# Optimization experiments

Measured on AMD Instinct MI355X. Metric: run time of the kernel, lower is better.

The kernel has to match this reference:

```python
import jax, jax.numpy as jnp
import numpy as np


def _orthogonalize(Wfree):
    # Wfree: (S, C, C) free parameters -> batched QR with sign correction
    Q, R = jnp.linalg.qr(Wfree)
    s = jnp.sign(jnp.diagonal(R, axis1=-2, axis2=-1))  # (S, C)
    s = jnp.where(s == 0, jnp.ones_like(s), s)
    return Q * s[:, None, :]  # column-wise sign fix


def _channel_mix(x, Wfree):
    # x: (B, C, H, W); Wfree: (H*W, C, C)
    B, C, H, Wd = x.shape
    S = H * Wd
    Q = _orthogonalize(Wfree)                      # (S, C, C)
    xr = x.reshape(B, C, S).transpose(0, 2, 1)     # (B, S, C)
    # y[b,s,:] = x[b,s,:] @ Q[s].T  (matches torch matmul(x, Q.T))
    y = jnp.einsum('bsk,sck->bsc', xr, Q)
    return y.transpose(0, 2, 1).reshape(B, C, H, Wd)


def setup_inputs() -> dict:
    key = jax.random.key(0)
    k0, k1, k2, k3 = jax.random.split(key, 4)
    init_scale = 0.001
    x0 = jax.random.normal(k0, (32, 64, 28, 28), dtype=jnp.float32)
    x1 = jax.random.normal(k1, (32, 256, 14, 14), dtype=jnp.float32)
    W0 = jax.random.normal(k2, (28 * 28, 64, 64), dtype=jnp.float32) * init_scale
    W1 = jax.random.normal(k3, (14 * 14, 256, 256), dtype=jnp.float32) * init_scale
    return {"x0": x0, "x1": x1, "W0": W0, "W1": W1}


def reference(x0, x1, W0, W1):
    # C=64 and C=256 are perfect squares, so channel padding is a no-op.
    y0 = _channel_mix(x0, W0)
    y1 = _channel_mix(x1, W1)
    return (y0, y1)
```

## Files before the change

kernel.cpp:

```cpp
#include <hip/hip_runtime.h>


static constexpr int BB = 32;

#define SCHED_FENCE() __builtin_amdgcn_sched_barrier(0)

template<int CTRL>
__device__ __forceinline__ float dpp_add(float x) {
    int y = __builtin_amdgcn_update_dpp(0, __float_as_int(x), CTRL, 0xF, 0xF, false);
    return x + __int_as_float(y);
}
__device__ __forceinline__ float rowred16(float p) {
    p = dpp_add<0x128>(p);
    p = dpp_add<0x124>(p);
    p = dpp_add<0x122>(p);
    p = dpp_add<0x121>(p);
    return p;
}

__device__ __forceinline__ int qoff(int j, int g, int r16) {
    return j * 256 + g * 64 + ((r16 ^ (2 * g)) << 2);
}

__global__ __launch_bounds__(256) void tkern(const float* __restrict__ in,
                                             float* __restrict__ out,
                                             int R, int S) {
    __shared__ float tile[32][33];
    const int tx = threadIdx.x, ty = threadIdx.y;
    const int s0 = blockIdx.x * 32, r0 = blockIdx.y * 32;
    #pragma unroll
    for (int i = ty; i < 32; i += 8) {
        int r = r0 + i, s = s0 + tx;
        tile[i][tx] = (r < R && s < S) ? in[(size_t)r * S + s] : 0.f;
    }
    __syncthreads();
    #pragma unroll
    for (int i = ty; i < 32; i += 8) {
        int s = s0 + i, r = r0 + tx;
        if (s < S && r < R) out[(size_t)s * R + r] = tile[tx][i];
    }
}

template<int C, int CT, int KC>
__device__ __forceinline__ void qr_body(const float* __restrict__ W,
                                        float* __restrict__ XY) {
    constexpr int RT = 16;
    constexpr int TR = C / RT;
    constexpr int THREADS = RT * CT;
    constexpr int QSTR = TR + 4;
    constexpr int XSTR = C + 4;

    const int s  = blockIdx.x;
    const int t  = threadIdx.x;
    const int rb = t & 15;
    const int cb = t >> 4;

    __shared__ float qs[2][RT * QSTR];
    __shared__ float xs[BB * XSTR];
    __shared__ float qc[KC * C];

    float a[TR][4];
    {
        const float* Wp = W + (size_t)s * C * C + (size_t)(rb * TR) * C + cb * 4;
        #pragma unroll
        for (int i = 0; i < TR; ++i) {
            float4 v = *reinterpret_cast<const float4*>(Wp + (size_t)i * C);
            a[i][0] = v.x; a[i][1] = v.y; a[i][2] = v.z; a[i][3] = v.w;
        }
    }
    {
        const float* Xp = XY + (size_t)s * BB * C;
        #pragma unroll
        for (int v = 0; v < (BB * C) / (4 * THREADS); ++v) {
            int idx = 4 * (t + v * THREADS);
            int b = idx / C, k = idx % C;
            float4 x4 = *reinterpret_cast<const float4*>(Xp + idx);
            *reinterpret_cast<float4*>(&xs[b * XSTR + k]) = x4;
        }
    }

    int buf = 0;
    #pragma unroll 1
    for (int j = 0; j < C; ++j) {
        const int cbj = j >> 2, jj = j & 3;
        if (cb == cbj) {
            #pragma unroll
            for (int q = 0; q < 4; ++q) {
                if (q == jj) {
                    float p = 0.f;
                    #pragma unroll
                    for (int i = 0; i < TR; ++i) p += a[i][q] * a[i][q];
                    p = rowred16(p);
                    const float rn = 1.0f / sqrtf(p);
                    #pragma unroll
                    for (int i = 0; i < TR; ++i) a[i][q] *= rn;
                    #pragma unroll
                    for (int i = 0; i < TR; i += 4) {
                        *reinterpret_cast<float4*>(&qs[buf][rb * QSTR + i]) =
                            make_float4(a[i][q], a[i+1][q], a[i+2][q], a[i+3][q]);
                    }
                }
            }
        }
        __syncthreads();
        if (cb * 4 + 3 > j) {
            float qv[TR];
            #pragma unroll
            for (int i = 0; i < TR; i += 4) {
                float4 v = *reinterpret_cast<const float4*>(&qs[buf][rb * QSTR + i]);
                qv[i] = v.x; qv[i+1] = v.y; qv[i+2] = v.z; qv[i+3] = v.w;
            }
            #pragma unroll
            for (int q = 0; q < 4; ++q) {
                if (cb * 4 + q > j) {
                    float p = 0.f;
                    #pragma unroll
                    for (int i = 0; i < TR; ++i) p += a[i][q] * qv[i];
                    p = rowred16(p);
                    #pragma unroll
                    for (int i = 0; i < TR; ++i) a[i][q] -= p * qv[i];
                }
            }
        }
        buf ^= 1;
    }

    const int u  = t % (C / 4);
    const int bp = t / (C / 4);
    float acc[2][4] = {{0,0,0,0},{0,0,0,0}};

    #pragma unroll 1
    for (int ch = 0; ch < C / KC; ++ch) {
        __syncthreads();
        if (cb >= (ch * KC) / 4 && cb < ((ch + 1) * KC) / 4) {
            #pragma unroll
            for (int q = 0; q < 4; ++q) {
                const int kk = cb * 4 + q - ch * KC;
                const int swz = (kk & 7) << 2;
                #pragma unroll
                for (int i = 0; i < TR; i += 4) {
                    const int cout = rb * TR + i;
                    *reinterpret_cast<float4*>(&qc[kk * C + (cout ^ swz)]) =
                        make_float4(a[i][q], a[i+1][q], a[i+2][q], a[i+3][q]);
                }
            }
        }
        __syncthreads();
        #pragma unroll
        for (int kk = 0; kk < KC; kk += 4) {
            const int k = ch * KC + kk;
            float4 x0 = *reinterpret_cast<const float4*>(&xs[(2*bp    ) * XSTR + k]);
            float4 x1 = *reinterpret_cast<const float4*>(&xs[(2*bp + 1) * XSTR + k]);
            #pragma unroll
            for (int m = 0; m < 4; ++m) {
                const int swz = ((kk + m) & 7) << 2;
                float4 qv4 = *reinterpret_cast<const float4*>(&qc[(kk + m) * C + ((4 * u) ^ swz)]);
                const float xa = (&x0.x)[m], xb = (&x1.x)[m];
                acc[0][0] += xa * qv4.x; acc[0][1] += xa * qv4.y;
                acc[0][2] += xa * qv4.z; acc[0][3] += xa * qv4.w;
                acc[1][0] += xb * qv4.x; acc[1][1] += xb * qv4.y;
                acc[1][2] += xb * qv4.z; acc[1][3] += xb * qv4.w;
            }
        }
    }
    {
        float* Yp = XY + (size_t)s * BB * C;
        *reinterpret_cast<float4*>(Yp + (2*bp    ) * C + 4 * u) =
            make_float4(acc[0][0], acc[0][1], acc[0][2], acc[0][3]);
        *reinterpret_cast<float4*>(Yp + (2*bp + 1) * C + 4 * u) =
            make_float4(acc[1][0], acc[1][1], acc[1][2], acc[1][3]);
    }
}

__global__ __launch_bounds__(256) void qr64(const float* __restrict__ W,
                                            float* __restrict__ XY) {
    qr_body<64, 16, 64>(W, XY);
}


__device__ __forceinline__ void dot_upd(float (&a)[2][16], const float* qpan,
                                        int j, int rb) {
    const float4 q40 = *reinterpret_cast<const float4*>(&qpan[qoff(j, 0, rb)]);
    const float4 q41 = *reinterpret_cast<const float4*>(&qpan[qoff(j, 1, rb)]);
    const float4 q42 = *reinterpret_cast<const float4*>(&qpan[qoff(j, 2, rb)]);
    const float4 q43 = *reinterpret_cast<const float4*>(&qpan[qoff(j, 3, rb)]);
    float p0 = 0.f, p1 = 0.f;
    p0 += a[0][ 0]*q40.x; p1 += a[1][ 0]*q40.x;
    p0 += a[0][ 1]*q40.y; p1 += a[1][ 1]*q40.y;
    p0 += a[0][ 2]*q40.z; p1 += a[1][ 2]*q40.z;
    p0 += a[0][ 3]*q40.w; p1 += a[1][ 3]*q40.w;
    p0 += a[0][ 4]*q41.x; p1 += a[1][ 4]*q41.x;
    p0 += a[0][ 5]*q41.y; p1 += a[1][ 5]*q41.y;
    p0 += a[0][ 6]*q41.z; p1 += a[1][ 6]*q41.z;
    p0 += a[0][ 7]*q41.w; p1 += a[1][ 7]*q41.w;
    p0 += a[0][ 8]*q42.x; p1 += a[1][ 8]*q42.x;
    p0 += a[0][ 9]*q42.y; p1 += a[1][ 9]*q42.y;
    p0 += a[0][10]*q42.z; p1 += a[1][10]*q42.z;
    p0 += a[0][11]*q42.w; p1 += a[1][11]*q42.w;
    p0 += a[0][12]*q43.x; p1 += a[1][12]*q43.x;
    p0 += a[0][13]*q43.y; p1 += a[1][13]*q43.y;
    p0 += a[0][14]*q43.z; p1 += a[1][14]*q43.z;
    p0 += a[0][15]*q43.w; p1 += a[1][15]*q43.w;
    p0 = rowred16(p0); p1 = rowred16(p1);
    a[0][ 0] -= p0*q40.x; a[0][ 1] -= p0*q40.y;
    a[0][ 2] -= p0*q40.z; a[0][ 3] -= p0*q40.w;
    a[0][ 4] -= p0*q41.x; a[0][ 5] -= p0*q41.y;
    a[0][ 6] -= p0*q41.z; a[0][ 7] -= p0*q41.w;
    a[0][ 8] -= p0*q42.x; a[0][ 9] -= p0*q42.y;
    a[0][10] -= p0*q42.z; a[0][11] -= p0*q42.w;
    a[0][12] -= p0*q43.x; a[0][13] -= p0*q43.y;
    a[0][14] -= p0*q43.z; a[0][15] -= p0*q43.w;
    a[1][ 0] -= p1*q40.x; a[1][ 1] -= p1*q40.y;
    a[1][ 2] -= p1*q40.z; a[1][ 3] -= p1*q40.w;
    a[1][ 4] -= p1*q41.x; a[1][ 5] -= p1*q41.y;
    a[1][ 6] -= p1*q41.z; a[1][ 7] -= p1*q41.w;
    a[1][ 8] -= p1*q42.x; a[1][ 9] -= p1*q42.y;
    a[1][10] -= p1*q42.z; a[1][11] -= p1*q42.w;
    a[1][12] -= p1*q43.x; a[1][13] -= p1*q43.y;
    a[1][14] -= p1*q43.z; a[1][15] -= p1*q43.w;
}

__device__ __forceinline__ void mini_mgs2(float (&a)[2][16], float* qpan,
                                          int jx, int rb) {
    float p = 0.f;
    #pragma unroll
    for (int i = 0; i < 16; ++i) p += a[0][i] * a[0][i];
    p = rowred16(p);
    float rn = 1.0f / sqrtf(p);
    #pragma unroll
    for (int i = 0; i < 16; ++i) a[0][i] *= rn;
    #pragma unroll
    for (int g = 0; g < 4; ++g) {
        *reinterpret_cast<float4*>(&qpan[qoff(jx, g, rb)]) =
            make_float4(a[0][4*g], a[0][4*g+1], a[0][4*g+2], a[0][4*g+3]);
    }
    float q = 0.f;
    #pragma unroll
    for (int i = 0; i < 16; ++i) q += a[1][i] * a[0][i];
    q = rowred16(q);
    #pragma unroll
    for (int i = 0; i < 16; ++i) a[1][i] -= q * a[0][i];
    p = 0.f;
    #pragma unroll
    for (int i = 0; i < 16; ++i) p += a[1][i] * a[1][i];
    p = rowred16(p);
    rn = 1.0f / sqrtf(p);
    #pragma unroll
    for (int i = 0; i < 16; ++i) a[1][i] *= rn;
    #pragma unroll
    for (int g = 0; g < 4; ++g) {
        *reinterpret_cast<float4*>(&qpan[qoff(jx + 1, g, rb)]) =
            make_float4(a[1][4*g], a[1][4*g+1], a[1][4*g+2], a[1][4*g+3]);
    }
}

__device__ __forceinline__ void apply1(float (&y0)[4], float (&y1)[4],
                                       const float* qpan, const float* xsb,
                                       int j, int u, int v) {
    float4 q4 = *reinterpret_cast<const float4*>(&qpan[qoff(j, u & 3, u >> 2)]);
    const float xa = xsb[j*33 + 2*v];
    const float xb = xsb[j*33 + 2*v + 1];
    y0[0] += xa*q4.x; y0[1] += xa*q4.y; y0[2] += xa*q4.z; y0[3] += xa*q4.w;
    y1[0] += xb*q4.x; y1[1] += xb*q4.y; y1[2] += xb*q4.z; y1[3] += xb*q4.w;
}

__device__ void panel_mgs(float (&a)[2][16], float (&y0)[4], float (&y1)[4],
                          float* qpan, const float* xsb,
                          int rb, int cb, int u, int v) {
    if (cb == 0) mini_mgs2(a, qpan, 0, rb);
    __syncthreads();
    #pragma unroll 1
    for (int m = 0; m < 64; ++m) {
        apply1(y0, y1, qpan, xsb, 2*m,     u, v);
        apply1(y0, y1, qpan, xsb, 2*m + 1, u, v);
        SCHED_FENCE();
        if (cb > m) {
            dot_upd(a, qpan, 2*m,     rb);
            SCHED_FENCE();
            dot_upd(a, qpan, 2*m + 1, rb);
            SCHED_FENCE();
            if (cb == m + 1) mini_mgs2(a, qpan, 2*m + 2, rb);
        }
        __syncthreads();
    }
}

__global__ __launch_bounds__(1024) void qr256ll(const float* __restrict__ W,
                                                float* __restrict__ XY) {
    __shared__ float qpan[128 * 256];
    __shared__ float xsb[128 * 33];

    const int s  = blockIdx.x;
    const int t  = threadIdx.x;
    const int rb = t & 15;
    const int cb = t >> 4;
    const int u  = t & 63;
    const int v  = t >> 6;

    const float* Wp = W + (size_t)s * 65536;
    float* Xp = XY + (size_t)s * 8192;

    float a[2][16];
    float y0[4] = {0,0,0,0};
    float y1[4] = {0,0,0,0};

    #pragma unroll
    for (int i = 0; i < 16; ++i) {
        float2 w2 = *reinterpret_cast<const float2*>(
            Wp + (size_t)(rb*16 + i) * 256 + 2*cb);
        a[0][i] = w2.x; a[1][i] = w2.y;
    }
    {
        const int tj = t & 127, tb = t >> 7;
        #pragma unroll
        for (int d = 0; d < 4; ++d)
            xsb[tj*33 + 4*tb + d] = Xp[(4*tb + d)*256 + tj];
    }
    panel_mgs(a, y0, y1, qpan, xsb, rb, cb, u, v);

    __syncthreads();
    #pragma unroll
    for (int i = 0; i < 16; ++i) {
        float2 w2 = *reinterpret_cast<const float2*>(
            Wp + (size_t)(rb*16 + i) * 256 + 128 + 2*cb);
        a[0][i] = w2.x; a[1][i] = w2.y;
    }
    {
        const int tj = t & 127, tb = t >> 7;
        #pragma unroll
        for (int d = 0; d < 4; ++d)
            xsb[tj*33 + 4*tb + d] = Xp[(4*tb + d)*256 + 128 + tj];
    }
    #pragma unroll 1
    for (int k = 0; k < 128; ++k) {
        dot_upd(a, qpan, k, rb);
        SCHED_FENCE();
    }
    __syncthreads();

    panel_mgs(a, y0, y1, qpan, xsb, rb, cb, u, v);

    *reinterpret_cast<float4*>(Xp + (size_t)(2*v    )*256 + 4*u) =
        make_float4(y0[0], y0[1], y0[2], y0[3]);
    *reinterpret_cast<float4*>(Xp + (size_t)(2*v + 1)*256 + 4*u) =
        make_float4(y1[0], y1[1], y1[2], y1[3]);
}

extern "C" void kernel_launch(void* const* d_in, const int* in_sizes, int n_in,
                              void* d_out, int out_size, void* d_ws, size_t ws_size,
                              hipStream_t stream) {
    (void)in_sizes; (void)n_in; (void)out_size; (void)ws_size;
    const float* x0 = (const float*)d_in[0];
    const float* x1 = (const float*)d_in[1];
    const float* W0 = (const float*)d_in[2];
    const float* W1 = (const float*)d_in[3];
    float* y0  = (float*)d_out;
    float* y1  = y0 + 1605632;
    float* xt0 = (float*)d_ws;
    float* xt1 = xt0 + 1605632;

    dim3 tb(32, 8);
    tkern<<<dim3(25,  64), tb, 0, stream>>>(x0, xt0, 2048, 784);
    tkern<<<dim3(7,  256), tb, 0, stream>>>(x1, xt1, 8192, 196);
    qr64   <<<784,  256, 0, stream>>>(W0, xt0);
    qr256ll<<<196, 1024, 0, stream>>>(W1, xt1);
    tkern<<<dim3(64,  25), tb, 0, stream>>>(xt0, y0, 784, 2048);
    tkern<<<dim3(256,  7), tb, 0, stream>>>(xt1, y1, 196, 8192);
}
```

Baseline: 288.7 us.

## Fuse the C=64 and C=256 QR kernels into one heterogeneous launch

```diff
diff --git a/kernel.cpp b/kernel.cpp
--- a/kernel.cpp
+++ b/kernel.cpp
@@ -43,25 +43,24 @@
 
 template<int C, int CT, int KC>
 __device__ __forceinline__ void qr_body(const float* __restrict__ W,
-                                        float* __restrict__ XY) {
+                                        float* __restrict__ XY,
+                                        float* __restrict__ sm, int t) {
     constexpr int RT = 16;
     constexpr int TR = C / RT;
     constexpr int THREADS = RT * CT;
     constexpr int QSTR = TR + 4;
     constexpr int XSTR = C + 4;
 
-    const int s  = blockIdx.x;
-    const int t  = threadIdx.x;
+    float* qs = sm;
+    float* xs = sm + 2 * RT * QSTR;
+    float* qc = xs + BB * XSTR;
+
     const int rb = t & 15;
     const int cb = t >> 4;
 
-    __shared__ float qs[2][RT * QSTR];
-    __shared__ float xs[BB * XSTR];
-    __shared__ float qc[KC * C];
-
     float a[TR][4];
     {
-        const float* Wp = W + (size_t)s * C * C + (size_t)(rb * TR) * C + cb * 4;
+        const float* Wp = W + (size_t)(rb * TR) * C + cb * 4;
         #pragma unroll
         for (int i = 0; i < TR; ++i) {
             float4 v = *reinterpret_cast<const float4*>(Wp + (size_t)i * C);
@@ -69,12 +68,11 @@
         }
     }
     {
-        const float* Xp = XY + (size_t)s * BB * C;
         #pragma unroll
         for (int v = 0; v < (BB * C) / (4 * THREADS); ++v) {
             int idx = 4 * (t + v * THREADS);
             int b = idx / C, k = idx % C;
-            float4 x4 = *reinterpret_cast<const float4*>(Xp + idx);
+            float4 x4 = *reinterpret_cast<const float4*>(XY + idx);
             *reinterpret_cast<float4*>(&xs[b * XSTR + k]) = x4;
         }
     }
@@ -96,7 +94,7 @@
                     for (int i = 0; i < TR; ++i) a[i][q] *= rn;
                     #pragma unroll
                     for (int i = 0; i < TR; i += 4) {
-                        *reinterpret_cast<float4*>(&qs[buf][rb * QSTR + i]) =
+                        *reinterpret_cast<float4*>(&qs[buf * RT * QSTR + rb * QSTR + i]) =
                             make_float4(a[i][q], a[i+1][q], a[i+2][q], a[i+3][q]);
                     }
                 }
@@ -107,7 +105,7 @@
             float qv[TR];
             #pragma unroll
             for (int i = 0; i < TR; i += 4) {
-                float4 v = *reinterpret_cast<const float4*>(&qs[buf][rb * QSTR + i]);
+                float4 v = *reinterpret_cast<const float4*>(&qs[buf * RT * QSTR + rb * QSTR + i]);
                 qv[i] = v.x; qv[i+1] = v.y; qv[i+2] = v.z; qv[i+3] = v.w;
             }
             #pragma unroll
@@ -164,19 +162,12 @@
         }
     }
     {
-        float* Yp = XY + (size_t)s * BB * C;
-        *reinterpret_cast<float4*>(Yp + (2*bp    ) * C + 4 * u) =
+        *reinterpret_cast<float4*>(XY + (2*bp    ) * C + 4 * u) =
             make_float4(acc[0][0], acc[0][1], acc[0][2], acc[0][3]);
-        *reinterpret_cast<float4*>(Yp + (2*bp + 1) * C + 4 * u) =
+        *reinterpret_cast<float4*>(XY + (2*bp + 1) * C + 4 * u) =
             make_float4(acc[1][0], acc[1][1], acc[1][2], acc[1][3]);
     }
 }
-
-__global__ __launch_bounds__(256) void qr64(const float* __restrict__ W,
-                                            float* __restrict__ XY) {
-    qr_body<64, 16, 64>(W, XY);
-}
-
 
 __device__ __forceinline__ void dot_upd(float (&a)[2][16], const float* qpan,
                                         int j, int rb) {
@@ -285,21 +276,17 @@
     }
 }
 
-__global__ __launch_bounds__(1024) void qr256ll(const float* __restrict__ W,
-                                                float* __restrict__ XY) {
-    __shared__ float qpan[128 * 256];
-    __shared__ float xsb[128 * 33];
-
-    const int s  = blockIdx.x;
-    const int t  = threadIdx.x;
+__device__ __forceinline__ void qr256_site(const float* __restrict__ Wp,
+                                           float* __restrict__ Xp,
+                                           float* __restrict__ sm, int t) {
+    float* qpan = sm;
+    float* xsb  = sm + 32768;
+
     const int rb = t & 15;
     const int cb = t >> 4;
     const int u  = t & 63;
     const int v  = t >> 6;
 
-    const float* Wp = W + (size_t)s * 65536;
-    float* Xp = XY + (size_t)s * 8192;
-
     float a[2][16];
     float y0[4] = {0,0,0,0};
     float y1[4] = {0,0,0,0};
@@ -344,6 +331,31 @@
         make_float4(y0[0], y0[1], y0[2], y0[3]);
     *reinterpret_cast<float4*>(Xp + (size_t)(2*v + 1)*256 + 4*u) =
         make_float4(y1[0], y1[1], y1[2], y1[3]);
+}
+
+static constexpr int SM64 = 2*16*8 + 32*68 + 64*64;
+
+__global__ __launch_bounds__(1024) void qr_all(const float* __restrict__ W0,
+                                               const float* __restrict__ W1,
+                                               float* __restrict__ XY0,
+                                               float* __restrict__ XY1) {
+    __shared__ float sm[32768 + 128*33];
+    const int bid = blockIdx.x;
+    const int t   = threadIdx.x;
+    if (bid < 196) {
+        qr256_site(W1 + (size_t)bid * 65536, XY1 + (size_t)bid * 8192, sm, t);
+    } else {
+        const int sl = t >> 8;
+        const int tt = t & 255;
+        float* smL = sm + sl * SM64;
+        #pragma unroll 1
+        for (int uu = bid - 196; uu < 196; uu += 60) {
+            const int site = 4 * uu + sl;
+            qr_body<64, 16, 64>(W0 + (size_t)site * 4096,
+                                XY0 + (size_t)site * 2048, smL, tt);
+            __syncthreads();
+        }
+    }
 }
 
 extern "C" void kernel_launch(void* const* d_in, const int* in_sizes, int n_in,
@@ -362,8 +374,7 @@
     dim3 tb(32, 8);
     tkern<<<dim3(25,  64), tb, 0, stream>>>(x0, xt0, 2048, 784);
     tkern<<<dim3(7,  256), tb, 0, stream>>>(x1, xt1, 8192, 196);
-    qr64   <<<784,  256, 0, stream>>>(W0, xt0);
-    qr256ll<<<196, 1024, 0, stream>>>(W1, xt1);
+    qr_all<<<256, 1024, 0, stream>>>(W0, W1, xt0, xt1);
     tkern<<<dim3(64,  25), tb, 0, stream>>>(xt0, y0, 784, 2048);
     tkern<<<dim3(256,  7), tb, 0, stream>>>(xt1, y1, 196, 8192);
 }
```

Result: faster. 250.1 us (median of 2 runs) (-13.4%).
